# Performance work log

Hardware: AMD Instinct MI355X
Metric: run time of the kernel (lower is better)

Reference implementation:

```python
import jax, jax.numpy as jnp
import numpy as np
import math

NUM_HEADS = 16

def setup_inputs() -> dict:
    key = jax.random.key(0)
    ks = jax.random.split(key, 5)
    d_model = 1024
    std = math.sqrt(2.0 / (d_model + d_model))
    x = jax.random.normal(ks[0], (2, 2048, d_model), dtype=jnp.float32)
    Wq = jax.random.normal(ks[1], (d_model, d_model), dtype=jnp.float32) * std
    Wk = jax.random.normal(ks[2], (d_model, d_model), dtype=jnp.float32) * std
    Wv = jax.random.normal(ks[3], (d_model, d_model), dtype=jnp.float32) * std
    Wo = jax.random.normal(ks[4], (d_model, d_model), dtype=jnp.float32) * std
    return {"x": x, "Wq": Wq, "Wk": Wk, "Wv": Wv, "Wo": Wo}

def reference(x, Wq, Wk, Wv, Wo):
    # x: [b, s, d]; W*: [d_out, d_in]
    b, s, d = x.shape
    h = NUM_HEADS
    dh = d // h
    def proj(W):
        y = jnp.einsum('bsd,ed->bse', x, W)           # [b, s, d]
        return y.reshape(b, s, h, dh).transpose(0, 2, 1, 3)  # [b, h, s, dh]
    Q, K, V = proj(Wq), proj(Wk), proj(Wv)
    scale = 1.0 / math.sqrt(dh)
    logits = jnp.einsum('bhqd,bhkd->bhqk', Q, K) * scale  # [b, h, s, s]
    causal = jnp.tril(jnp.ones((s, s), dtype=bool))
    logits = jnp.where(causal, logits, -jnp.inf)
    attn = jax.nn.softmax(logits, axis=-1)
    out = jnp.einsum('bhqk,bhkd->bhqd', attn, V)          # [b, h, s, dh]
    out = out.transpose(0, 2, 1, 3).reshape(b, s, d)
    return jnp.einsum('bsv,dv->bsd', out, Wo)
```

## Files before the change

kernel.cpp:

```cpp
#include <hip/hip_runtime.h>
#include <hip/hip_bf16.h>
#include <math.h>

typedef unsigned short ushort_t;
typedef __attribute__((ext_vector_type(8))) short bf16x8;
typedef __attribute__((ext_vector_type(4))) float f32x4;

#define MFMA16(a,b,c) __builtin_amdgcn_mfma_f32_16x16x32_bf16(a,b,c,0,0,0)
#define QSCALE 0.1803368801111204f

typedef unsigned int u32;
typedef __attribute__((address_space(1))) const u32* gp1_t;
typedef __attribute__((address_space(3))) u32* lp3_t;

__device__ __forceinline__ void async_copy16(void* l, const void* g) {
    __builtin_amdgcn_global_load_lds((gp1_t)g, (lp3_t)l, 16, 0, 0);
}

__device__ __forceinline__ ushort_t f2bf(float f) {
    unsigned u = __float_as_uint(f);
    unsigned r = u + 0x7fffu + ((u >> 16) & 1u);
    return (ushort_t)(r >> 16);
}

__global__ __launch_bounds__(256) void cvt_kernel(
    const float* __restrict__ x,  const float* __restrict__ wq,
    const float* __restrict__ wk, const float* __restrict__ wv,
    const float* __restrict__ wo, ushort_t* __restrict__ dst)
{
    size_t base = ((size_t)blockIdx.x * 256 + threadIdx.x) * 8;
    const float* src; size_t off;
    if      (base < 4194304ul) { src = x;  off = base; }
    else if (base < 5242880ul) { src = wq; off = base - 4194304ul; }
    else if (base < 6291456ul) { src = wk; off = base - 5242880ul; }
    else if (base < 7340032ul) { src = wv; off = base - 6291456ul; }
    else                       { src = wo; off = base - 7340032ul; }
    float4 a = *(const float4*)(src + off);
    float4 b = *(const float4*)(src + off + 4);
    struct alignas(16) U8 { ushort_t v[8]; } o;
    o.v[0]=f2bf(a.x); o.v[1]=f2bf(a.y); o.v[2]=f2bf(a.z); o.v[3]=f2bf(a.w);
    o.v[4]=f2bf(b.x); o.v[5]=f2bf(b.y); o.v[6]=f2bf(b.z); o.v[7]=f2bf(b.w);
    *(U8*)(dst + base) = o;
}

__global__ __launch_bounds__(512) void gemm_bt(
    const ushort_t* __restrict__ A, const ushort_t* __restrict__ B,
    ushort_t* __restrict__ Oq, ushort_t* __restrict__ Ok,
    ushort_t* __restrict__ Ovt, float* __restrict__ Of, int is_out)
{
    __shared__ ushort_t As[2][128 * 64];
    __shared__ ushort_t Bs[2][128 * 64];
    const int t = threadIdx.x, l = t & 63, w = t >> 6;
    const int l4 = l >> 4, lm = l & 15;
    const int wr = w >> 1, wc = w & 1;

    const int nwg = gridDim.x * gridDim.y;
    const int orig = (int)blockIdx.y * gridDim.x + (int)blockIdx.x;
    const int qq = nwg >> 3;
    const int swz = (orig & 7) * qq + (orig >> 3);
    const int n0 = (swz % gridDim.x) * 128;
    const int m0 = (swz / gridDim.x) * 128;

    const int srow = t >> 3, scol = t & 7;

    f32x4 acc[2][4] = {};

    #pragma unroll
    for (int i = 0; i < 2; ++i) {
        const int row = i * 64 + srow;
        const int c = scol ^ (row & 7);
        async_copy16((char*)&As[0][0] + i * 8192 + t * 16,
                     A + (size_t)(m0 + row) * 1024 + c * 8);
        async_copy16((char*)&Bs[0][0] + i * 8192 + t * 16,
                     B + (size_t)(n0 + row) * 1024 + c * 8);
    }

    for (int kt = 0; kt < 16; ++kt) {
        const int cur = kt & 1;
        if (kt + 1 < 16) {
            const int k0 = (kt + 1) * 64;
            #pragma unroll
            for (int i = 0; i < 2; ++i) {
                const int row = i * 64 + srow;
                const int c = scol ^ (row & 7);
                async_copy16((char*)&As[cur ^ 1][0] + i * 8192 + t * 16,
                             A + (size_t)(m0 + row) * 1024 + k0 + c * 8);
                async_copy16((char*)&Bs[cur ^ 1][0] + i * 8192 + t * 16,
                             B + (size_t)(n0 + row) * 1024 + k0 + c * 8);
            }
            asm volatile("s_waitcnt vmcnt(4)" ::: "memory");
        } else {
            asm volatile("s_waitcnt vmcnt(0)" ::: "memory");
        }
        __builtin_amdgcn_s_barrier();

        #pragma unroll
        for (int ks = 0; ks < 2; ++ks) {
            bf16x8 af[2], bfr[4];
            #pragma unroll
            for (int mi = 0; mi < 2; ++mi) {
                const int row = wr * 32 + mi * 16 + lm;
                const int ch = l4 + 4 * ks;
                af[mi] = *(const bf16x8*)(&As[cur][0] + row * 64 + ((ch ^ (row & 7)) << 3));
            }
            #pragma unroll
            for (int ni = 0; ni < 4; ++ni) {
                const int row = wc * 64 + ni * 16 + lm;
                const int ch = l4 + 4 * ks;
                bfr[ni] = *(const bf16x8*)(&Bs[cur][0] + row * 64 + ((ch ^ (row & 7)) << 3));
            }
            #pragma unroll
            for (int mi = 0; mi < 2; ++mi)
                #pragma unroll
                for (int ni = 0; ni < 4; ++ni)
                    acc[mi][ni] = MFMA16(af[mi], bfr[ni], acc[mi][ni]);
        }
        asm volatile("s_waitcnt lgkmcnt(0)" ::: "memory");
        __builtin_amdgcn_s_barrier();
    }

    const int mb = m0 + wr * 32, nb = n0 + wc * 64;
    if (is_out) {
        #pragma unroll
        for (int mi = 0; mi < 2; ++mi)
            #pragma unroll
            for (int ni = 0; ni < 4; ++ni) {
                const int n = nb + ni * 16 + lm;
                const int mr = mb + mi * 16 + l4 * 4;
                #pragma unroll
                for (int r = 0; r < 4; ++r)
                    Of[(size_t)(mr + r) * 1024 + n] = acc[mi][ni][r];
            }
    } else if (nb >= 2048) {
        #pragma unroll
        for (int mi = 0; mi < 2; ++mi)
            #pragma unroll
            for (int ni = 0; ni < 4; ++ni) {
                const int nv = nb - 2048 + ni * 16 + lm;
                const int m = mb + mi * 16 + l4 * 4;
                const int b = m >> 11, s = m & 2047, h = nv >> 6, d = nv & 63;
                ushort4 pk;
                pk.x = f2bf(acc[mi][ni][0]); pk.y = f2bf(acc[mi][ni][1]);
                pk.z = f2bf(acc[mi][ni][2]); pk.w = f2bf(acc[mi][ni][3]);
                *(ushort4*)(Ovt + (((size_t)(b * 16 + h) * 64 + d) * 2048 + s)) = pk;
            }
    } else {
        ushort_t* O = (nb < 1024) ? Oq : Ok;
        const float qs = (nb < 1024) ? (float)QSCALE : 1.0f;
        const int nbase = nb & 1023;
        #pragma unroll
        for (int mi = 0; mi < 2; ++mi)
            #pragma unroll
            for (int ni = 0; ni < 4; ++ni) {
                const int n = nbase + ni * 16 + lm;
                const int h = n >> 6, d = n & 63;
                #pragma unroll
                for (int r = 0; r < 4; ++r) {
                    const int m = mb + mi * 16 + l4 * 4 + r;
                    const int b = m >> 11, s = m & 2047;
                    O[((size_t)(b * 16 + h) * 2048 + s) * 64 + d] =
                        f2bf(acc[mi][ni][r] * qs);
                }
            }
    }
}

template<bool MASK>
__device__ __forceinline__ void attn_tile(
    const ushort_t* Kbuf, const ushort_t* Vbuf, ushort_t* Pw,
    const bf16x8 (&qf)[2][2], const bf16x8 ones,
    f32x4 (&o)[2][4], f32x4 (&ol)[2], float (&m_run)[2],
    int kv0, int q0w, int l4, int lm)
{
    f32x4 sf[2][4] = {};
    #pragma unroll
    for (int ks = 0; ks < 2; ++ks)
        #pragma unroll
        for (int cf = 0; cf < 4; ++cf) {
            const int rowK = cf * 16 + lm;
            const int ch = l4 + 4 * ks;
            bf16x8 kf = *(const bf16x8*)(Kbuf + rowK * 64 + ((ch ^ (rowK & 7)) << 3));
            sf[0][cf] = MFMA16(kf, qf[0][ks], sf[0][cf]);
            sf[1][cf] = MFMA16(kf, qf[1][ks], sf[1][cf]);
        }

    float tmax[2] = {-1e30f, -1e30f};
    #pragma unroll
    for (int qi = 0; qi < 2; ++qi) {
        const int qrow = q0w + qi * 16 + lm;
        #pragma unroll
        for (int cf = 0; cf < 4; ++cf)
            #pragma unroll
            for (int r = 0; r < 4; ++r) {
                float v = sf[qi][cf][r];
                if (MASK && (kv0 + cf * 16 + l4 * 4 + r > qrow)) v = -30000.f;
                sf[qi][cf][r] = v;
                tmax[qi] = fmaxf(tmax[qi], v);
            }
        tmax[qi] = fmaxf(tmax[qi], __shfl_xor(tmax[qi], 16));
        tmax[qi] = fmaxf(tmax[qi], __shfl_xor(tmax[qi], 32));
    }

    if (!__all(fmaxf(tmax[0] - m_run[0], tmax[1] - m_run[1]) <= 8.f)) {
        #pragma unroll
        for (int qi = 0; qi < 2; ++qi) {
            const float mn = fmaxf(m_run[qi], tmax[qi]);
            const float alpha = __builtin_amdgcn_exp2f(m_run[qi] - mn);
            #pragma unroll
            for (int df = 0; df < 4; ++df)
                #pragma unroll
                for (int r = 0; r < 4; ++r)
                    o[qi][df][r] *= alpha;
            #pragma unroll
            for (int r = 0; r < 4; ++r) ol[qi][r] *= alpha;
            m_run[qi] = mn;
        }
    }

    #pragma unroll
    for (int qi = 0; qi < 2; ++qi)
        #pragma unroll
        for (int cf = 0; cf < 4; ++cf) {
            float p0 = __builtin_amdgcn_exp2f(sf[qi][cf][0] - m_run[qi]);
            float p1 = __builtin_amdgcn_exp2f(sf[qi][cf][1] - m_run[qi]);
            float p2 = __builtin_amdgcn_exp2f(sf[qi][cf][2] - m_run[qi]);
            float p3 = __builtin_amdgcn_exp2f(sf[qi][cf][3] - m_run[qi]);
            __hip_bfloat162 b01 = __float22bfloat162_rn(make_float2(p0, p1));
            __hip_bfloat162 b23 = __float22bfloat162_rn(make_float2(p2, p3));
            uint2 pkv;
            __builtin_memcpy(&pkv.x, &b01, 4);
            __builtin_memcpy(&pkv.y, &b23, 4);
            *(uint2*)&Pw[(qi * 16 + lm) * 72 + cf * 16 + l4 * 4] = pkv;
        }

    #pragma unroll
    for (int ks = 0; ks < 2; ++ks) {
        bf16x8 pf0 = *(const bf16x8*)&Pw[(0 * 16 + lm) * 72 + ks * 32 + l4 * 8];
        bf16x8 pf1 = *(const bf16x8*)&Pw[(1 * 16 + lm) * 72 + ks * 32 + l4 * 8];
        #pragma unroll
        for (int df = 0; df < 4; ++df) {
            const int rowV = df * 16 + lm;
            const int ch = l4 + 4 * ks;
            bf16x8 vf = *(const bf16x8*)(Vbuf + rowV * 64 + ((ch ^ (rowV & 7)) << 3));
            o[0][df] = MFMA16(vf, pf0, o[0][df]);
            o[1][df] = MFMA16(vf, pf1, o[1][df]);
        }
        ol[0] = MFMA16(ones, pf0, ol[0]);
        ol[1] = MFMA16(ones, pf1, ol[1]);
    }
}

__global__ __launch_bounds__(256) void attn_kernel(
    const ushort_t* __restrict__ Qg, const ushort_t* __restrict__ Kg,
    const ushort_t* __restrict__ Vtg, ushort_t* __restrict__ Og)
{
    __shared__ ushort_t Ks[2][64 * 64];
    __shared__ ushort_t Vs[2][64 * 64];
    __shared__ ushort_t Ps[4][32 * 72];
    const int t = threadIdx.x, l = t & 63, w = t >> 6;
    const int l4 = l >> 4, lm = l & 15;
    const int bh = blockIdx.x;
    const int qt = 15 - (int)blockIdx.y;
    const int q0 = qt * 128, q0w = q0 + w * 32;

    bf16x8 qf[2][2];
    #pragma unroll
    for (int qi = 0; qi < 2; ++qi) {
        const ushort_t* qp = Qg + ((size_t)bh * 2048 + q0w + qi * 16 + lm) * 64 + l4 * 8;
        qf[qi][0] = *(const bf16x8*)qp;
        qf[qi][1] = *(const bf16x8*)(qp + 32);
    }
    bf16x8 ones;
    #pragma unroll
    for (int i = 0; i < 8; ++i) ones[i] = (short)0x3F80;

    f32x4 o[2][4] = {};
    f32x4 ol[2] = {};
    float m_run[2] = {-1e30f, -1e30f};

    const int nkv = 2 * qt + 2;
    const int srow = t >> 3, scol = t & 7;
    const ushort_t* kg0 = Kg + ((size_t)bh * 2048 + srow) * 64 + (scol ^ (srow & 7)) * 8;
    const ushort_t* vg0 = Vtg + ((size_t)bh * 64 + srow) * 2048 + (scol ^ (srow & 7)) * 8;

    async_copy16((char*)&Ks[0][0] + t * 16, kg0);
    async_copy16((char*)&Vs[0][0] + t * 16, vg0);
    async_copy16((char*)&Ks[0][0] + 4096 + t * 16, kg0 + 32 * 64);
    async_copy16((char*)&Vs[0][0] + 4096 + t * 16, vg0 + 32 * 2048);
    __syncthreads();

    int kt = 0;
    for (; kt < nkv - 2; ++kt) {
        const int cur = kt & 1;
        const size_t koff = (size_t)(kt + 1) * 64 * 64;
        const size_t voff = (size_t)(kt + 1) * 64;
        async_copy16((char*)&Ks[cur ^ 1][0] + t * 16, kg0 + koff);
        async_copy16((char*)&Vs[cur ^ 1][0] + t * 16, vg0 + voff);
        async_copy16((char*)&Ks[cur ^ 1][0] + 4096 + t * 16, kg0 + koff + 32 * 64);
        async_copy16((char*)&Vs[cur ^ 1][0] + 4096 + t * 16, vg0 + voff + 32 * 2048);

        attn_tile<false>(&Ks[cur][0], &Vs[cur][0], &Ps[w][0],
                         qf, ones, o, ol, m_run, kt * 64, q0w, l4, lm);
        __syncthreads();
    }
    for (; kt < nkv; ++kt) {
        const int cur = kt & 1;
        if (kt + 1 < nkv) {
            const size_t koff = (size_t)(kt + 1) * 64 * 64;
            const size_t voff = (size_t)(kt + 1) * 64;
            async_copy16((char*)&Ks[cur ^ 1][0] + t * 16, kg0 + koff);
            async_copy16((char*)&Vs[cur ^ 1][0] + t * 16, vg0 + voff);
            async_copy16((char*)&Ks[cur ^ 1][0] + 4096 + t * 16, kg0 + koff + 32 * 64);
            async_copy16((char*)&Vs[cur ^ 1][0] + 4096 + t * 16, vg0 + voff + 32 * 2048);
        }
        attn_tile<true>(&Ks[cur][0], &Vs[cur][0], &Ps[w][0],
                        qf, ones, o, ol, m_run, kt * 64, q0w, l4, lm);
        __syncthreads();
    }

    const int b = bh >> 4, h = bh & 15;
    #pragma unroll
    for (int qi = 0; qi < 2; ++qi) {
        const float inv = 1.f / ol[qi][0];
        const int srow_o = q0w + qi * 16 + lm;
        #pragma unroll
        for (int df = 0; df < 4; ++df) {
            ushort4 pk4;
            pk4.x = f2bf(o[qi][df][0] * inv); pk4.y = f2bf(o[qi][df][1] * inv);
            pk4.z = f2bf(o[qi][df][2] * inv); pk4.w = f2bf(o[qi][df][3] * inv);
            *(ushort4*)&Og[((size_t)(b * 2048 + srow_o)) * 1024 + h * 64 + df * 16 + l4 * 4] = pk4;
        }
    }
}

extern "C" void kernel_launch(void* const* d_in, const int* in_sizes, int n_in,
                              void* d_out, int out_size, void* d_ws, size_t ws_size,
                              hipStream_t stream)
{
    const float* x  = (const float*)d_in[0];
    const float* Wq = (const float*)d_in[1];
    const float* Wk = (const float*)d_in[2];
    const float* Wv = (const float*)d_in[3];
    const float* Wo = (const float*)d_in[4];

    ushort_t* ws  = (ushort_t*)d_ws;
    ushort_t* xb  = ws;
    ushort_t* wqb = ws + 4194304;
    ushort_t* wob = ws + 7340032;
    ushort_t* Qw  = ws + 8388608;
    ushort_t* Kw  = ws + 12582912;
    ushort_t* Vtw = ws + 16777216;
    ushort_t* Aow = ws + 20971520;

    cvt_kernel<<<4096, 256, 0, stream>>>(x, Wq, Wk, Wv, Wo, ws);
    gemm_bt<<<dim3(24, 32), 512, 0, stream>>>(xb, wqb, Qw, Kw, Vtw, nullptr, 0);
    attn_kernel<<<dim3(32, 16), 256, 0, stream>>>(Qw, Kw, Vtw, Aow);
    gemm_bt<<<dim3(8, 32), 512, 0, stream>>>(Aow, wob, nullptr, nullptr, nullptr,
                                             (float*)d_out, 1);
}
```

Measured before the change: 117.4 us.

## Split KV range across two warp groups in attention with LSE merge

The attention block grows from 256 to 512 threads. Two groups of four waves each process alternating KV tiles for the same 128 query rows, and their partial outputs, row sums and running maxima are merged through shared memory at the end. This shortens each block's serial KV loop and adds in-flight waves to hide latency. In exchange it uses more LDS, adds raw barriers with manual waitcnt, and pays a final merge step.

```diff
diff --git a/kernel.cpp b/kernel.cpp
--- a/kernel.cpp
+++ b/kernel.cpp
@@ -166,7 +166,7 @@
 }
 
 template<bool MASK>
-__device__ __forceinline__ void attn_tile(
+__device__ __forceinline__ void attn_tile2(
     const ushort_t* Kbuf, const ushort_t* Vbuf, ushort_t* Pw,
     const bf16x8 (&qf)[2][2], const bf16x8 ones,
     f32x4 (&o)[2][4], f32x4 (&ol)[2], float (&m_run)[2],
@@ -250,18 +250,24 @@
     }
 }
 
-__global__ __launch_bounds__(256) void attn_kernel(
+__global__ __launch_bounds__(512) void attn_kernel(
     const ushort_t* __restrict__ Qg, const ushort_t* __restrict__ Kg,
     const ushort_t* __restrict__ Vtg, ushort_t* __restrict__ Og)
 {
-    __shared__ ushort_t Ks[2][64 * 64];
-    __shared__ ushort_t Vs[2][64 * 64];
-    __shared__ ushort_t Ps[4][32 * 72];
+    __shared__ ushort_t smem[51200];
+    ushort_t* Ksm = smem;
+    ushort_t* Vsm = smem + 16384;
+    ushort_t* Psm = smem + 32768;
+
     const int t = threadIdx.x, l = t & 63, w = t >> 6;
     const int l4 = l >> 4, lm = l & 15;
+    const int kvg = w >> 2, qg = w & 3;
     const int bh = blockIdx.x;
     const int qt = 15 - (int)blockIdx.y;
-    const int q0 = qt * 128, q0w = q0 + w * 32;
+    const int q0 = qt * 128, q0w = q0 + qg * 32;
+
+    const ushort_t* Kbh = Kg + (size_t)bh * 2048 * 64;
+    const ushort_t* Vbh = Vtg + (size_t)bh * 64 * 2048;
 
     bf16x8 qf[2][2];
     #pragma unroll
@@ -278,57 +284,97 @@
     f32x4 ol[2] = {};
     float m_run[2] = {-1e30f, -1e30f};
 
-    const int nkv = 2 * qt + 2;
-    const int srow = t >> 3, scol = t & 7;
-    const ushort_t* kg0 = Kg + ((size_t)bh * 2048 + srow) * 64 + (scol ^ (srow & 7)) * 8;
-    const ushort_t* vg0 = Vtg + ((size_t)bh * 64 + srow) * 2048 + (scol ^ (srow & 7)) * 8;
-
-    async_copy16((char*)&Ks[0][0] + t * 16, kg0);
-    async_copy16((char*)&Vs[0][0] + t * 16, vg0);
-    async_copy16((char*)&Ks[0][0] + 4096 + t * 16, kg0 + 32 * 64);
-    async_copy16((char*)&Vs[0][0] + 4096 + t * 16, vg0 + 32 * 2048);
+    const int tg = t & 255;
+    const int sr0 = tg >> 3, sc0 = tg & 7;
+    const ushort_t* kp[2]; const ushort_t* vp[2];
+    char* kd[2]; char* vd[2];
+    #pragma unroll
+    for (int i = 0; i < 2; ++i) {
+        const int row = i * 32 + sr0;
+        const int c = sc0 ^ (row & 7);
+        kp[i] = Kbh + row * 64 + c * 8;
+        vp[i] = Vbh + (size_t)row * 2048 + c * 8;
+        kd[i] = (char*)Ksm + kvg * 16384 + i * 4096 + tg * 16;
+        vd[i] = (char*)Vsm + kvg * 16384 + i * 4096 + tg * 16;
+    }
+    ushort_t* Pw = Psm + w * 2304;
+    const ushort_t* Kgrp = Ksm + kvg * 8192;
+    const ushort_t* Vgrp = Vsm + kvg * 8192;
+
+    const int nst = qt + 1;
+    {
+        const int kv0p = kvg * 64;
+        #pragma unroll
+        for (int i = 0; i < 2; ++i) {
+            async_copy16(kd[i], kp[i] + (size_t)kv0p * 64);
+            async_copy16(vd[i], vp[i] + kv0p);
+        }
+    }
+
+    for (int s = 0; s < nst; ++s) {
+        const int cur = s & 1;
+        if (s + 1 < nst) {
+            const int kv0n = (2 * (s + 1) + kvg) * 64;
+            #pragma unroll
+            for (int i = 0; i < 2; ++i) {
+                async_copy16(kd[i] + (cur ^ 1) * 8192, kp[i] + (size_t)kv0n * 64);
+                async_copy16(vd[i] + (cur ^ 1) * 8192, vp[i] + kv0n);
+            }
+            asm volatile("s_waitcnt vmcnt(4)" ::: "memory");
+        } else {
+            asm volatile("s_waitcnt vmcnt(0)" ::: "memory");
+        }
+        __builtin_amdgcn_s_barrier();
+
+        const int kv0 = (2 * s + kvg) * 64;
+        if ((s + 1 < nst) || (q0w + 31 >= kv0)) {
+            if (s + 1 < nst)
+                attn_tile2<false>(Kgrp + cur * 4096, Vgrp + cur * 4096, Pw,
+                                  qf, ones, o, ol, m_run, kv0, q0w, l4, lm);
+            else
+                attn_tile2<true>(Kgrp + cur * 4096, Vgrp + cur * 4096, Pw,
+                                 qf, ones, o, ol, m_run, kv0, q0w, l4, lm);
+        }
+        asm volatile("s_waitcnt lgkmcnt(0)" ::: "memory");
+        __builtin_amdgcn_s_barrier();
+    }
+
+    float* sc = (float*)smem;
+    const int mb_ = (qg * 64 + l) * 37;
+    if (kvg == 1) {
+        #pragma unroll
+        for (int qi = 0; qi < 2; ++qi) {
+            #pragma unroll
+            for (int df = 0; df < 4; ++df)
+                #pragma unroll
+                for (int r = 0; r < 4; ++r)
+                    sc[mb_ + qi * 18 + df * 4 + r] = o[qi][df][r];
+            sc[mb_ + qi * 18 + 16] = ol[qi][0];
+            sc[mb_ + qi * 18 + 17] = m_run[qi];
+        }
+    }
     __syncthreads();
-
-    int kt = 0;
-    for (; kt < nkv - 2; ++kt) {
-        const int cur = kt & 1;
-        const size_t koff = (size_t)(kt + 1) * 64 * 64;
-        const size_t voff = (size_t)(kt + 1) * 64;
-        async_copy16((char*)&Ks[cur ^ 1][0] + t * 16, kg0 + koff);
-        async_copy16((char*)&Vs[cur ^ 1][0] + t * 16, vg0 + voff);
-        async_copy16((char*)&Ks[cur ^ 1][0] + 4096 + t * 16, kg0 + koff + 32 * 64);
-        async_copy16((char*)&Vs[cur ^ 1][0] + 4096 + t * 16, vg0 + voff + 32 * 2048);
-
-        attn_tile<false>(&Ks[cur][0], &Vs[cur][0], &Ps[w][0],
-                         qf, ones, o, ol, m_run, kt * 64, q0w, l4, lm);
-        __syncthreads();
-    }
-    for (; kt < nkv; ++kt) {
-        const int cur = kt & 1;
-        if (kt + 1 < nkv) {
-            const size_t koff = (size_t)(kt + 1) * 64 * 64;
-            const size_t voff = (size_t)(kt + 1) * 64;
-            async_copy16((char*)&Ks[cur ^ 1][0] + t * 16, kg0 + koff);
-            async_copy16((char*)&Vs[cur ^ 1][0] + t * 16, vg0 + voff);
-            async_copy16((char*)&Ks[cur ^ 1][0] + 4096 + t * 16, kg0 + koff + 32 * 64);
-            async_copy16((char*)&Vs[cur ^ 1][0] + 4096 + t * 16, vg0 + voff + 32 * 2048);
-        }
-        attn_tile<true>(&Ks[cur][0], &Vs[cur][0], &Ps[w][0],
-                        qf, ones, o, ol, m_run, kt * 64, q0w, l4, lm);
-        __syncthreads();
-    }
-
-    const int b = bh >> 4, h = bh & 15;
-    #pragma unroll
-    for (int qi = 0; qi < 2; ++qi) {
-        const float inv = 1.f / ol[qi][0];
-        const int srow_o = q0w + qi * 16 + lm;
-        #pragma unroll
-        for (int df = 0; df < 4; ++df) {
-            ushort4 pk4;
-            pk4.x = f2bf(o[qi][df][0] * inv); pk4.y = f2bf(o[qi][df][1] * inv);
-            pk4.z = f2bf(o[qi][df][2] * inv); pk4.w = f2bf(o[qi][df][3] * inv);
-            *(ushort4*)&Og[((size_t)(b * 2048 + srow_o)) * 1024 + h * 64 + df * 16 + l4 * 4] = pk4;
+    if (kvg == 0) {
+        const int b = bh >> 4, h = bh & 15;
+        #pragma unroll
+        for (int qi = 0; qi < 2; ++qi) {
+            const float mB = sc[mb_ + qi * 18 + 17];
+            const float lB = sc[mb_ + qi * 18 + 16];
+            const float m = fmaxf(m_run[qi], mB);
+            const float aA = __builtin_amdgcn_exp2f(m_run[qi] - m);
+            const float aB = __builtin_amdgcn_exp2f(mB - m);
+            const float inv = 1.f / (ol[qi][0] * aA + lB * aB);
+            const int srow_o = q0w + qi * 16 + lm;
+            #pragma unroll
+            for (int df = 0; df < 4; ++df) {
+                ushort4 pk4;
+                float v0 = (o[qi][df][0] * aA + sc[mb_ + qi * 18 + df * 4 + 0] * aB) * inv;
+                float v1 = (o[qi][df][1] * aA + sc[mb_ + qi * 18 + df * 4 + 1] * aB) * inv;
+                float v2 = (o[qi][df][2] * aA + sc[mb_ + qi * 18 + df * 4 + 2] * aB) * inv;
+                float v3 = (o[qi][df][3] * aA + sc[mb_ + qi * 18 + df * 4 + 3] * aB) * inv;
+                pk4.x = f2bf(v0); pk4.y = f2bf(v1); pk4.z = f2bf(v2); pk4.w = f2bf(v3);
+                *(ushort4*)&Og[((size_t)(b * 2048 + srow_o)) * 1024 + h * 64 + df * 16 + l4 * 4] = pk4;
+            }
         }
     }
 }
@@ -354,7 +400,7 @@
 
     cvt_kernel<<<4096, 256, 0, stream>>>(x, Wq, Wk, Wv, Wo, ws);
     gemm_bt<<<dim3(24, 32), 512, 0, stream>>>(xb, wqb, Qw, Kw, Vtw, nullptr, 0);
-    attn_kernel<<<dim3(32, 16), 256, 0, stream>>>(Qw, Kw, Vtw, Aow);
+    attn_kernel<<<dim3(32, 16), 512, 0, stream>>>(Qw, Kw, Vtw, Aow);
     gemm_bt<<<dim3(8, 32), 512, 0, stream>>>(Aow, wob, nullptr, nullptr, nullptr,
                                              (float*)d_out, 1);
 }
```

Measured after the change: 105.9 us. 1.11x faster.
